# Optimization experiments

Hardware: AMD Instinct MI355X
Metric: run time of the kernel (lower is better)

The kernel has to match this reference:

```python
import jax, jax.numpy as jnp
import numpy as np

NEG = -1e30   # finite stand-in for -inf (keeps vjp NaN-free)
BLANK = 0


def _ctc_loss_mean(logits, targets):
    """CTC loss matching torch.nn.CTCLoss(blank=0, zero_infinity=True,
    reduction='mean') applied to log_softmax(logits).permute(1,0,2), with
    input_lengths = T and uniform target_lengths = L.

    logits:  (B, T, K) raw scores
    targets: (B, L) int labels in [1, K) (no blanks)
    """
    B, T, K = logits.shape
    L = targets.shape[1]
    S = 2 * L + 1  # extended label sequence: blank-interleaved

    logp = jax.nn.log_softmax(logits, axis=-1)  # (B, T, K)

    # extended labels ext = [blank, y1, blank, y2, ..., yL, blank]
    ext = jnp.full((B, S), BLANK, dtype=targets.dtype)
    ext = ext.at[:, 1::2].set(targets)  # (B, S)

    # per-step log-probs of extended labels: lp[b, t, s] = logp[b, t, ext[b, s]]
    lp = jnp.take_along_axis(logp, ext[:, None, :], axis=2)  # (B, T, S)

    # skip transition (s-2 -> s) allowed iff ext[s] != blank and ext[s] != ext[s-2]
    skip = jnp.concatenate(
        [jnp.zeros((B, 2), dtype=bool),
         (ext[:, 2:] != BLANK) & (ext[:, 2:] != ext[:, :-2])], axis=1)  # (B, S)

    # alpha init at t = 0
    alpha0 = jnp.full((B, S), NEG, dtype=logp.dtype)
    alpha0 = alpha0.at[:, 0].set(lp[:, 0, 0]).at[:, 1].set(lp[:, 0, 1])

    pad1 = jnp.full((B, 1), NEG, dtype=logp.dtype)
    pad2 = jnp.full((B, 2), NEG, dtype=logp.dtype)

    def step(alpha, lp_t):
        a1 = alpha                                            # stay
        a2 = jnp.concatenate([pad1, alpha[:, :-1]], axis=1)   # advance 1
        a3 = jnp.concatenate([pad2, alpha[:, :-2]], axis=1)   # advance 2
        a3 = jnp.where(skip, a3, NEG)
        new = jnp.logaddexp(jnp.logaddexp(a1, a2), a3) + lp_t
        return new, None

    xs = jnp.swapaxes(lp[:, 1:, :], 0, 1)  # (T-1, B, S)
    alpha, _ = jax.lax.scan(step, alpha0, xs)

    # total log-likelihood: end at last blank or last label
    logl = jnp.logaddexp(alpha[:, S - 1], alpha[:, S - 2])  # (B,)

    per = -logl / L  # 'mean' reduction divides each loss by target length
    per = jnp.where(logl > -1e29, per, 0.0)  # zero_infinity
    return jnp.mean(per)


def setup_inputs() -> dict:
    key = jax.random.key(0)
    k1, k2 = jax.random.split(key)
    B, T, K, L = 64, 1024, 512, 100
    logits = jax.random.normal(k1, (B, T, K), dtype=jnp.float32)
    targets = jax.random.randint(k2, (B, L), 1, K)  # labels exclude blank=0
    return {"logits": logits, "targets": targets}


def reference(logits, targets):
    return _ctc_loss_mean(logits, targets)
```

## Files before the change

kernel.cpp:

```cpp
#include <hip/hip_runtime.h>
#include <hip/hip_fp16.h>


#define TT 1024
#define BB 64
#define KK 512
#define LL 100

static constexpr float L2E = 1.44269504088896340736f;
static constexpr float LN2 = 0.69314718055994530942f;

__device__ __forceinline__ float dpp_shr1_z(float x) {
  return __builtin_bit_cast(float,
      __builtin_amdgcn_update_dpp(0, __builtin_bit_cast(int, x),
                                  0x138, 0xf, 0xf, true));
}
__device__ __forceinline__ int dpp_shr1_zi(int x) {
  return __builtin_amdgcn_update_dpp(0, x, 0x138, 0xf, 0xf, true);
}

__device__ __forceinline__ float slog2(float x) {
  return x > 0.0f ? log2f(x) : -1.0e30f;
}

__device__ __forceinline__ float2 upk(unsigned u) {
  return __half22float2(__builtin_bit_cast(__half2, u));
}

__global__ __launch_bounds__(256) void k_probs(const float* __restrict__ logits,
                                               const int* __restrict__ targets,
                                               unsigned* __restrict__ pk,
                                               float* __restrict__ lbArr,
                                               float* __restrict__ out) {
  const int wid = threadIdx.x >> 6;
  const int lane = threadIdx.x & 63;
  const int row = (blockIdx.x << 2) + wid;
  const int b = row >> 10;
  const float* x = logits + (size_t)row * KK;

  if (blockIdx.x == 0 && threadIdx.x == 0) out[0] = 0.0f;

  __shared__ float sx[4][KK];

  const float4 v0 = reinterpret_cast<const float4*>(x)[lane];
  const float4 v1 = reinterpret_cast<const float4*>(x)[lane + 64];
  float4* sp = reinterpret_cast<float4*>(sx[wid]);
  sp[lane] = v0;
  sp[lane + 64] = v1;

  float m = fmaxf(fmaxf(fmaxf(v0.x, v0.y), fmaxf(v0.z, v0.w)),
                  fmaxf(fmaxf(v1.x, v1.y), fmaxf(v1.z, v1.w)));
  #pragma unroll
  for (int d = 1; d < 64; d <<= 1) m = fmaxf(m, __shfl_xor(m, d));

  float e = exp2f((v0.x - m) * L2E) + exp2f((v0.y - m) * L2E) +
            exp2f((v0.z - m) * L2E) + exp2f((v0.w - m) * L2E) +
            exp2f((v1.x - m) * L2E) + exp2f((v1.y - m) * L2E) +
            exp2f((v1.z - m) * L2E) + exp2f((v1.w - m) * L2E);
  #pragma unroll
  for (int d = 1; d < 64; d <<= 1) e += __shfl_xor(e, d);

  __syncthreads();
  const float xb = sx[wid][0];

  float ox = 0.0f, oy = 0.0f;
  if (lane >= 1 && lane <= 50) {
    const int2 c = *reinterpret_cast<const int2*>(
        targets + b * LL + (2 * lane - 2));
    ox = exp2f((sx[wid][c.x] - xb) * L2E);
    oy = exp2f((sx[wid][c.y] - xb) * L2E);
  }
  const int word = (lane == 0) ? 63 : (lane - 1);
  const __half2 h = __floats2half2_rn(ox, oy);
  pk[(size_t)(row >> 1) * 128 + word * 2 + (row & 1)] =
      __builtin_bit_cast(unsigned, h);

  if (lane == 0) lbArr[row] = (xb - m) * L2E + 9.0f - log2f(e);
}

__global__ __launch_bounds__(128) void k_ctc(const unsigned* __restrict__ pk,
                                             const float* __restrict__ lbArr,
                                             const int* __restrict__ targets,
                                             float* __restrict__ out) {
  const int b = blockIdx.x;
  const int lane = threadIdx.x & 63;
  const int wv = threadIdx.x >> 6;
  const int i = lane;
  const int* tg = targets + b * LL;

  __shared__ float sG[6][64];

  float S0 = 0.0f, S1 = 0.0f, S2 = 0.0f, S3 = 0.0f;
  int ea = 0;
  float f1 = 1.0f, f2 = 1.0f;

  const float4* lbv = reinterpret_cast<const float4*>(lbArr + (size_t)b * TT);
  const int lbbase = (wv == 0) ? 0 : 128;
  const float4 lb0 = lbv[lbbase + lane];
  const float4 lb1 = lbv[lbbase + lane + 64];

#define RESC()                                                             \
  do {                                                                     \
    const float m_ = fmaxf(fmaxf(S0, S1), fmaxf(S2, S3));                  \
    int E_ = (int)((__float_as_uint(m_) >> 23) & 255) - 127;               \
    E_ = (m_ > 0.0f) ? E_ : 0;                                             \
    const float sc_ = __uint_as_float((unsigned)(127 - E_) << 23);         \
    S0 *= sc_; S1 *= sc_; S2 *= sc_; S3 *= sc_;                            \
    ea += E_;                                                              \
    int dE_ = dpp_shr1_zi(ea) - ea;                                        \
    dE_ = dE_ < -250 ? -250 : (dE_ > 250 ? 250 : dE_);                     \
    const int h_ = dE_ / 2;                                                \
    f1 = __uint_as_float((unsigned)(127 + h_) << 23);                      \
    f2 = __uint_as_float((unsigned)(127 + (dE_ - h_)) << 23);              \
  } while (0)

  uint2 RA[8], RB[8], RC[8], RD[8], RE[8], RF[8], RG[8], RH[8];

  if (wv == 0) {
    const unsigned* gb = pk + (size_t)b * 512 * 128 + i * 2;
    float mA = 0.0f, mB = 0.0f;
    if (i > 0 && 2 * i <= LL - 1)
      mA = (tg[2 * i] != tg[2 * i - 1]) ? 1.0f : 0.0f;
    if (2 * i + 1 <= LL - 1)
      mB = (tg[2 * i + 1] != tg[2 * i]) ? 1.0f : 0.0f;
    S0 = (i == 0) ? 1.0f : 0.0f;

#define FISSUE(BUF, CHN)                                                   \
    do {                                                                   \
      if ((CHN) < 32) {                                                    \
        _Pragma("unroll") for (int j = 0; j < 8; ++j)                      \
          BUF[j] = *reinterpret_cast<const uint2*>(                        \
              gb + (size_t)((CHN) * 8 + j) * 128);                         \
        __builtin_amdgcn_sched_barrier(0);                                 \
      }                                                                    \
    } while (0)
#define FSTEP(R)                                                           \
    do {                                                                   \
      const float A3 = dpp_shr1_z(S3) * f1 * f2;                           \
      const float n0 = S0 + A3;                                            \
      const float n1 = (S0 + S1 + mA * A3) * (R).x;                        \
      const float n2 = S1 + S2;                                            \
      const float n3 = (S2 + S3 + mB * S1) * (R).y;                        \
      S0 = n0; S1 = n1; S2 = n2; S3 = n3;                                  \
    } while (0)
#define FCOMPUTE(BUF)                                                      \
    do {                                                                   \
      _Pragma("unroll") for (int j = 0; j < 8; ++j) {                      \
        const float2 re = upk(BUF[j].x);                                   \
        FSTEP(re);                                                         \
        const float2 ro = upk(BUF[j].y);                                   \
        FSTEP(ro);                                                         \
        if ((j & 3) == 3) RESC();                       \
      }                                                                    \
    } while (0)

    FISSUE(RA, 0); FISSUE(RB, 1); FISSUE(RC, 2); FISSUE(RD, 3);
    FISSUE(RE, 4); FISSUE(RF, 5); FISSUE(RG, 6);
    for (int c = 0; c < 32; c += 8) {
      FISSUE(RH, c + 7);  FCOMPUTE(RA);
      FISSUE(RA, c + 8);  FCOMPUTE(RB);
      FISSUE(RB, c + 9);  FCOMPUTE(RC);
      FISSUE(RC, c + 10); FCOMPUTE(RD);
      FISSUE(RD, c + 11); FCOMPUTE(RE);
      FISSUE(RE, c + 12); FCOMPUTE(RF);
      FISSUE(RF, c + 13); FCOMPUTE(RG);
      FISSUE(RG, c + 14); FCOMPUTE(RH);
    }
#undef FISSUE
#undef FSTEP
#undef FCOMPUTE
  } else {
    const int ii = 50 - i;
    const int w = (ii >= 0) ? ii : 50;
    const unsigned* gb = pk + (size_t)b * 512 * 128 + w * 2;
    float mBb = 0.0f, mAn = 0.0f;
    if (ii >= 0 && 2 * ii + 1 <= LL - 1)
      mBb = (tg[2 * ii + 1] != tg[2 * ii]) ? 1.0f : 0.0f;
    if (ii >= 0 && ii <= 48)
      mAn = (tg[2 * ii + 2] != tg[2 * ii + 1]) ? 1.0f : 0.0f;
    if (i == 0) S0 = 1.0f;
    if (i == 1) S3 = 1.0f;

#define BISSUE(BUF, CHN)                                                   \
    do {                                                                   \
      if ((CHN) < 32) {                                                    \
        _Pragma("unroll") for (int j = 0; j < 8; ++j)                      \
          BUF[j] = *reinterpret_cast<const uint2*>(                        \
              gb + (size_t)(511 - ((CHN) * 8 + j)) * 128);                 \
        __builtin_amdgcn_sched_barrier(0);                                 \
      }                                                                    \
    } while (0)
#define BSTEP(R)                                                           \
    do {                                                                   \
      const float s2 = dpp_shr1_z((R).x);           \
      const float H0 = dpp_shr1_z(S0) * f1 * f2;                           \
      const float H1 = dpp_shr1_z(S1) * f1 * f2;                           \
      const float u = (R).x * S1;                                          \
      const float v = (R).y * S3;                                          \
      const float n0 = S0 + u;                                             \
      const float n1 = u + fmaf(mBb, v, S2);                               \
      const float n2 = S2 + v;                                             \
      const float n3 = v + fmaf(mAn, s2 * H1, H0);                         \
      S0 = n0; S1 = n1; S2 = n2; S3 = n3;                                  \
    } while (0)
#define BCOMPUTE(BUF)                                                      \
    do {                                                                   \
      _Pragma("unroll") for (int j = 0; j < 8; ++j) {                      \
        const float2 ro = upk(BUF[j].y);                                   \
        BSTEP(ro);                                                         \
        const float2 re = upk(BUF[j].x);                                   \
        BSTEP(re);                                                         \
        if ((j & 3) == 3) RESC();                       \
      }                                                                    \
    } while (0)

    BISSUE(RA, 0); BISSUE(RB, 1); BISSUE(RC, 2); BISSUE(RD, 3);
    BISSUE(RE, 4); BISSUE(RF, 5); BISSUE(RG, 6);
    for (int c = 0; c < 32; c += 8) {
      BISSUE(RH, c + 7);  BCOMPUTE(RA);
      BISSUE(RA, c + 8);  BCOMPUTE(RB);
      BISSUE(RB, c + 9);  BCOMPUTE(RC);
      BISSUE(RC, c + 10); BCOMPUTE(RD);
      BISSUE(RD, c + 11); BCOMPUTE(RE);
      BISSUE(RE, c + 12); BCOMPUTE(RF);
      BISSUE(RF, c + 13); BCOMPUTE(RG);
      BISSUE(RG, c + 14); BCOMPUTE(RH);
    }
#undef BISSUE
#undef BSTEP
#undef BCOMPUTE
  }
#undef RESC

  float s4 = (lb0.x + lb0.y) + (lb0.z + lb0.w) +
             (lb1.x + lb1.y) + (lb1.z + lb1.w);
  #pragma unroll
  for (int d = 1; d < 64; d <<= 1) s4 += __shfl_xor(s4, d);

  if (wv == 1) {
    sG[0][lane] = S0; sG[1][lane] = S1; sG[2][lane] = S2; sG[3][lane] = S3;
    sG[4][lane] = (float)ea;
    if (lane == 0) sG[5][0] = s4;
  }

  __syncthreads();

  if (wv == 0) {
    const int gj = (i <= 50) ? (50 - i) : 63;
    const float eb = sG[4][gj];
    const float eff = (float)ea;
    float w0 = slog2(S0) + eff + slog2(sG[0][gj]) + eb;
    float w1 = slog2(S1) + eff + slog2(sG[1][gj]) + eb;
    float w2 = slog2(S2) + eff + slog2(sG[2][gj]) + eb;
    float w3 = slog2(S3) + eff + slog2(sG[3][gj]) + eb;
    float wm = fmaxf(fmaxf(w0, w1), fmaxf(w2, w3));
    #pragma unroll
    for (int d = 1; d < 64; d <<= 1) wm = fmaxf(wm, __shfl_xor(wm, d));
    float ss = exp2f(w0 - wm) + exp2f(w1 - wm) +
               exp2f(w2 - wm) + exp2f(w3 - wm);
    #pragma unroll
    for (int d = 1; d < 64; d <<= 1) ss += __shfl_xor(ss, d);

    if (i == 0) {
      const float lbsum = s4 + sG[5][0];
      float loss = 0.0f;
      if (wm > -1.0e29f) {
        const float logl2 = wm + log2f(ss) + lbsum - (float)(TT * 9);
        loss = -(logl2 * LN2) / (float)LL;
      }
      atomicAdd(out, loss * (1.0f / (float)BB));
    }
  }
}

extern "C" void kernel_launch(void* const* d_in, const int* in_sizes, int n_in,
                              void* d_out, int out_size, void* d_ws, size_t ws_size,
                              hipStream_t stream) {
  const float* logits = (const float*)d_in[0];
  const int* targets = (const int*)d_in[1];
  float* out = (float*)d_out;

  unsigned* pk = (unsigned*)d_ws;
  float* lbArr = (float*)d_ws + (size_t)BB * 512 * 128;

  hipLaunchKernelGGL(k_probs, dim3(BB * TT / 4), dim3(256), 0, stream,
                     logits, targets, pk, lbArr, out);
  hipLaunchKernelGGL(k_ctc, dim3(BB), dim3(128), 0, stream,
                     pk, lbArr, targets, out);
}
```

Baseline: 51.63 us.

## Split CTC recurrence across kernels to overlap it with middle-row softmax

The single probability kernel and the single recurrence kernel become three. The first computes edge time rows. The middle kernel runs the first 320 forward and backward steps while other blocks compute the softmax for the middle 384 rows. The tail kernel reloads the saved alpha/beta state and finishes the recurrence. This hides part of the serial recurrence behind memory-bound softmax work, at the cost of an extra launch, a state round-trip through global memory, and a shallower 4-buffer prefetch pipeline.

```diff
diff --git a/kernel.cpp b/kernel.cpp
--- a/kernel.cpp
+++ b/kernel.cpp
@@ -6,6 +6,7 @@
 #define BB 64
 #define KK 512
 #define LL 100
+#define DLT 320
 
 static constexpr float L2E = 1.44269504088896340736f;
 static constexpr float LN2 = 0.69314718055994530942f;
@@ -18,35 +19,141 @@
 __device__ __forceinline__ int dpp_shr1_zi(int x) {
   return __builtin_amdgcn_update_dpp(0, x, 0x138, 0xf, 0xf, true);
 }
-
 __device__ __forceinline__ float slog2(float x) {
   return x > 0.0f ? log2f(x) : -1.0e30f;
 }
-
 __device__ __forceinline__ float2 upk(unsigned u) {
   return __half22float2(__builtin_bit_cast(__half2, u));
 }
 
-__global__ __launch_bounds__(256) void k_probs(const float* __restrict__ logits,
-                                               const int* __restrict__ targets,
-                                               unsigned* __restrict__ pk,
-                                               float* __restrict__ lbArr,
-                                               float* __restrict__ out) {
-  const int wid = threadIdx.x >> 6;
-  const int lane = threadIdx.x & 63;
-  const int row = (blockIdx.x << 2) + wid;
-  const int b = row >> 10;
+__device__ __forceinline__ void resc(float& S0, float& S1, float& S2,
+                                     float& S3, int& ea, float& f1,
+                                     float& f2) {
+  const float m = fmaxf(fmaxf(S0, S1), fmaxf(S2, S3));
+  int E = (int)((__float_as_uint(m) >> 23) & 255) - 127;
+  E = (m > 0.0f) ? E : 0;
+  const float sc = __uint_as_float((unsigned)(127 - E) << 23);
+  S0 *= sc; S1 *= sc; S2 *= sc; S3 *= sc;
+  ea += E;
+  int dE = dpp_shr1_zi(ea) - ea;
+  dE = dE < -250 ? -250 : (dE > 250 ? 250 : dE);
+  const int h = dE / 2;
+  f1 = __uint_as_float((unsigned)(127 + h) << 23);
+  f2 = __uint_as_float((unsigned)(127 + (dE - h)) << 23);
+}
+__device__ __forceinline__ void refresh_f(int ea, float& f1, float& f2) {
+  int dE = dpp_shr1_zi(ea) - ea;
+  dE = dE < -250 ? -250 : (dE > 250 ? 250 : dE);
+  const int h = dE / 2;
+  f1 = __uint_as_float((unsigned)(127 + h) << 23);
+  f2 = __uint_as_float((unsigned)(127 + (dE - h)) << 23);
+}
+
+__device__ __forceinline__ void fstep(float2 r, float mA, float mB,
+                                      float& S0, float& S1, float& S2,
+                                      float& S3, float f1, float f2) {
+  const float A3 = dpp_shr1_z(S3) * f1 * f2;
+  const float n0 = S0 + A3;
+  const float n1 = (S0 + S1 + mA * A3) * r.x;
+  const float n2 = S1 + S2;
+  const float n3 = (S2 + S3 + mB * S1) * r.y;
+  S0 = n0; S1 = n1; S2 = n2; S3 = n3;
+}
+__device__ __forceinline__ void bstep(float2 r, float mBb, float mAn,
+                                      float& S0, float& S1, float& S2,
+                                      float& S3, float f1, float f2) {
+  const float s2 = dpp_shr1_z(r.x);
+  const float H0 = dpp_shr1_z(S0) * f1 * f2;
+  const float H1 = dpp_shr1_z(S1) * f1 * f2;
+  const float u = r.x * S1;
+  const float v = r.y * S3;
+  const float n0 = S0 + u;
+  const float n1 = u + fmaf(mBb, v, S2);
+  const float n2 = S2 + v;
+  const float n3 = v + fmaf(mAn, s2 * H1, H0);
+  S0 = n0; S1 = n1; S2 = n2; S3 = n3;
+}
+
+template <int CB, int NC>
+__device__ __forceinline__ void run_fwd(const unsigned* __restrict__ gb,
+                                        float mA, float mB, float& S0,
+                                        float& S1, float& S2, float& S3,
+                                        int& ea, float& f1, float& f2) {
+  uint2 RA[8], RB[8], RC[8], RD[8];
+#define ISSUE(BUF, CHN)                                                    \
+  do {                                                                     \
+    if ((CHN) < NC) {                                                      \
+      _Pragma("unroll") for (int j = 0; j < 8; ++j)                        \
+        BUF[j] = *reinterpret_cast<const uint2*>(                          \
+            gb + (size_t)((CB + (CHN)) * 8 + j) * 128);                    \
+      __builtin_amdgcn_sched_barrier(0);                                   \
+    }                                                                      \
+  } while (0)
+#define COMP(BUF)                                                          \
+  do {                                                                     \
+    _Pragma("unroll") for (int j = 0; j < 8; ++j) {                        \
+      fstep(upk(BUF[j].x), mA, mB, S0, S1, S2, S3, f1, f2);                \
+      fstep(upk(BUF[j].y), mA, mB, S0, S1, S2, S3, f1, f2);                \
+      if ((j & 3) == 3) resc(S0, S1, S2, S3, ea, f1, f2);                  \
+    }                                                                      \
+  } while (0)
+  ISSUE(RA, 0); ISSUE(RB, 1); ISSUE(RC, 2);
+  for (int c = 0; c < NC; c += 4) {
+    ISSUE(RD, c + 3); COMP(RA);
+    ISSUE(RA, c + 4); COMP(RB);
+    ISSUE(RB, c + 5); COMP(RC);
+    ISSUE(RC, c + 6); COMP(RD);
+  }
+#undef ISSUE
+#undef COMP
+}
+
+template <int CB, int NC>
+__device__ __forceinline__ void run_bwd(const unsigned* __restrict__ gb,
+                                        float mBb, float mAn, float& S0,
+                                        float& S1, float& S2, float& S3,
+                                        int& ea, float& f1, float& f2) {
+  uint2 RA[8], RB[8], RC[8], RD[8];
+#define ISSUE(BUF, CHN)                                                    \
+  do {                                                                     \
+    if ((CHN) < NC) {                                                      \
+      _Pragma("unroll") for (int j = 0; j < 8; ++j)                        \
+        BUF[j] = *reinterpret_cast<const uint2*>(                          \
+            gb + (size_t)(511 - ((CB + (CHN)) * 8 + j)) * 128);            \
+      __builtin_amdgcn_sched_barrier(0);                                   \
+    }                                                                      \
+  } while (0)
+#define COMP(BUF)                                                          \
+  do {                                                                     \
+    _Pragma("unroll") for (int j = 0; j < 8; ++j) {                        \
+      bstep(upk(BUF[j].y), mBb, mAn, S0, S1, S2, S3, f1, f2);              \
+      bstep(upk(BUF[j].x), mBb, mAn, S0, S1, S2, S3, f1, f2);              \
+      if ((j & 3) == 3) resc(S0, S1, S2, S3, ea, f1, f2);                  \
+    }                                                                      \
+  } while (0)
+  ISSUE(RA, 0); ISSUE(RB, 1); ISSUE(RC, 2);
+  for (int c = 0; c < NC; c += 4) {
+    ISSUE(RD, c + 3); COMP(RA);
+    ISSUE(RA, c + 4); COMP(RB);
+    ISSUE(RB, c + 5); COMP(RC);
+    ISSUE(RC, c + 6); COMP(RD);
+  }
+#undef ISSUE
+#undef COMP
+}
+
+__device__ __forceinline__ void prob_row(const float* __restrict__ logits,
+                                         const int* __restrict__ targets,
+                                         unsigned* __restrict__ pk,
+                                         float* __restrict__ lbArr,
+                                         int b, int t, int lane, float* sp) {
+  const int row = (b << 10) + t;
   const float* x = logits + (size_t)row * KK;
-
-  if (blockIdx.x == 0 && threadIdx.x == 0) out[0] = 0.0f;
-
-  __shared__ float sx[4][KK];
-
   const float4 v0 = reinterpret_cast<const float4*>(x)[lane];
   const float4 v1 = reinterpret_cast<const float4*>(x)[lane + 64];
-  float4* sp = reinterpret_cast<float4*>(sx[wid]);
-  sp[lane] = v0;
-  sp[lane + 64] = v1;
+  float4* sp4 = reinterpret_cast<float4*>(sp);
+  sp4[lane] = v0;
+  sp4[lane + 64] = v1;
 
   float m = fmaxf(fmaxf(fmaxf(v0.x, v0.y), fmaxf(v0.z, v0.w)),
                   fmaxf(fmaxf(v1.x, v1.y), fmaxf(v1.z, v1.w)));
@@ -61,116 +168,73 @@
   for (int d = 1; d < 64; d <<= 1) e += __shfl_xor(e, d);
 
   __syncthreads();
-  const float xb = sx[wid][0];
+  const float xb = sp[0];
 
   float ox = 0.0f, oy = 0.0f;
   if (lane >= 1 && lane <= 50) {
     const int2 c = *reinterpret_cast<const int2*>(
         targets + b * LL + (2 * lane - 2));
-    ox = exp2f((sx[wid][c.x] - xb) * L2E);
-    oy = exp2f((sx[wid][c.y] - xb) * L2E);
+    ox = exp2f((sp[c.x] - xb) * L2E);
+    oy = exp2f((sp[c.y] - xb) * L2E);
   }
   const int word = (lane == 0) ? 63 : (lane - 1);
   const __half2 h = __floats2half2_rn(ox, oy);
   pk[(size_t)(row >> 1) * 128 + word * 2 + (row & 1)] =
       __builtin_bit_cast(unsigned, h);
-
   if (lane == 0) lbArr[row] = (xb - m) * L2E + 9.0f - log2f(e);
 }
 
-__global__ __launch_bounds__(128) void k_ctc(const unsigned* __restrict__ pk,
-                                             const float* __restrict__ lbArr,
-                                             const int* __restrict__ targets,
-                                             float* __restrict__ out) {
-  const int b = blockIdx.x;
+__global__ __launch_bounds__(256) void k_probs_edge(
+    const float* __restrict__ logits, const int* __restrict__ targets,
+    unsigned* __restrict__ pk, float* __restrict__ lbArr,
+    float* __restrict__ out) {
+  if (blockIdx.x == 0 && threadIdx.x == 0) out[0] = 0.0f;
+  const int wid = threadIdx.x >> 6;
+  const int lane = threadIdx.x & 63;
+  __shared__ float sx[4][KK];
+  const int e = (blockIdx.x << 2) + wid;
+  const int b = e / 640;
+  const int w = e - b * 640;
+  const int t = (w < DLT) ? w : (TT - 640) + w;
+  prob_row(logits, targets, pk, lbArr, b, t, lane, sx[wid]);
+}
+
+__global__ __launch_bounds__(256) void k_mid(
+    const float* __restrict__ logits, const int* __restrict__ targets,
+    unsigned* __restrict__ pk, float* __restrict__ lbArr,
+    float* __restrict__ st) {
   const int lane = threadIdx.x & 63;
   const int wv = threadIdx.x >> 6;
-  const int i = lane;
+  __shared__ float sx[4][KK];
+
+  if (blockIdx.x >= BB) {
+    const int m = ((blockIdx.x - BB) << 2) + wv;
+    const int b = m / 384;
+    const int w = m - b * 384;
+    prob_row(logits, targets, pk, lbArr, b, DLT + w, lane, sx[wv]);
+    return;
+  }
+
+  if (wv >= 2) return;
+  const int b = blockIdx.x;
+  const int dir = wv;
   const int* tg = targets + b * LL;
-
-  __shared__ float sG[6][64];
 
   float S0 = 0.0f, S1 = 0.0f, S2 = 0.0f, S3 = 0.0f;
   int ea = 0;
   float f1 = 1.0f, f2 = 1.0f;
 
-  const float4* lbv = reinterpret_cast<const float4*>(lbArr + (size_t)b * TT);
-  const int lbbase = (wv == 0) ? 0 : 128;
-  const float4 lb0 = lbv[lbbase + lane];
-  const float4 lb1 = lbv[lbbase + lane + 64];
-
-#define RESC()                                                             \
-  do {                                                                     \
-    const float m_ = fmaxf(fmaxf(S0, S1), fmaxf(S2, S3));                  \
-    int E_ = (int)((__float_as_uint(m_) >> 23) & 255) - 127;               \
-    E_ = (m_ > 0.0f) ? E_ : 0;                                             \
-    const float sc_ = __uint_as_float((unsigned)(127 - E_) << 23);         \
-    S0 *= sc_; S1 *= sc_; S2 *= sc_; S3 *= sc_;                            \
-    ea += E_;                                                              \
-    int dE_ = dpp_shr1_zi(ea) - ea;                                        \
-    dE_ = dE_ < -250 ? -250 : (dE_ > 250 ? 250 : dE_);                     \
-    const int h_ = dE_ / 2;                                                \
-    f1 = __uint_as_float((unsigned)(127 + h_) << 23);                      \
-    f2 = __uint_as_float((unsigned)(127 + (dE_ - h_)) << 23);              \
-  } while (0)
-
-  uint2 RA[8], RB[8], RC[8], RD[8], RE[8], RF[8], RG[8], RH[8];
-
-  if (wv == 0) {
-    const unsigned* gb = pk + (size_t)b * 512 * 128 + i * 2;
+  if (dir == 0) {
+    const unsigned* gb = pk + (size_t)b * 512 * 128 + lane * 2;
     float mA = 0.0f, mB = 0.0f;
-    if (i > 0 && 2 * i <= LL - 1)
-      mA = (tg[2 * i] != tg[2 * i - 1]) ? 1.0f : 0.0f;
-    if (2 * i + 1 <= LL - 1)
-      mB = (tg[2 * i + 1] != tg[2 * i]) ? 1.0f : 0.0f;
-    S0 = (i == 0) ? 1.0f : 0.0f;
-
-#define FISSUE(BUF, CHN)                                                   \
-    do {                                                                   \
-      if ((CHN) < 32) {                                                    \
-        _Pragma("unroll") for (int j = 0; j < 8; ++j)                      \
-          BUF[j] = *reinterpret_cast<const uint2*>(                        \
-              gb + (size_t)((CHN) * 8 + j) * 128);                         \
-        __builtin_amdgcn_sched_barrier(0);                                 \
-      }                                                                    \
-    } while (0)
-#define FSTEP(R)                                                           \
-    do {                                                                   \
-      const float A3 = dpp_shr1_z(S3) * f1 * f2;                           \
-      const float n0 = S0 + A3;                                            \
-      const float n1 = (S0 + S1 + mA * A3) * (R).x;                        \
-      const float n2 = S1 + S2;                                            \
-      const float n3 = (S2 + S3 + mB * S1) * (R).y;                        \
-      S0 = n0; S1 = n1; S2 = n2; S3 = n3;                                  \
-    } while (0)
-#define FCOMPUTE(BUF)                                                      \
-    do {                                                                   \
-      _Pragma("unroll") for (int j = 0; j < 8; ++j) {                      \
-        const float2 re = upk(BUF[j].x);                                   \
-        FSTEP(re);                                                         \
-        const float2 ro = upk(BUF[j].y);                                   \
-        FSTEP(ro);                                                         \
-        if ((j & 3) == 3) RESC();                       \
-      }                                                                    \
-    } while (0)
-
-    FISSUE(RA, 0); FISSUE(RB, 1); FISSUE(RC, 2); FISSUE(RD, 3);
-    FISSUE(RE, 4); FISSUE(RF, 5); FISSUE(RG, 6);
-    for (int c = 0; c < 32; c += 8) {
-      FISSUE(RH, c + 7);  FCOMPUTE(RA);
-      FISSUE(RA, c + 8);  FCOMPUTE(RB);
-      FISSUE(RB, c + 9);  FCOMPUTE(RC);
-      FISSUE(RC, c + 10); FCOMPUTE(RD);
-      FISSUE(RD, c + 11); FCOMPUTE(RE);
-      FISSUE(RE, c + 12); FCOMPUTE(RF);
-      FISSUE(RF, c + 13); FCOMPUTE(RG);
-      FISSUE(RG, c + 14); FCOMPUTE(RH);
-    }
-#undef FISSUE
-#undef FSTEP
-#undef FCOMPUTE
+    if (lane > 0 && 2 * lane <= LL - 1)
+      mA = (tg[2 * lane] != tg[2 * lane - 1]) ? 1.0f : 0.0f;
+    if (2 * lane + 1 <= LL - 1)
+      mB = (tg[2 * lane + 1] != tg[2 * lane]) ? 1.0f : 0.0f;
+    S0 = (lane == 0) ? 1.0f : 0.0f;
+    run_fwd<0, 20>(gb, mA, mB, S0, S1, S2, S3, ea, f1, f2);
   } else {
-    const int ii = 50 - i;
+    const int ii = 50 - lane;
     const int w = (ii >= 0) ? ii : 50;
     const unsigned* gb = pk + (size_t)b * 512 * 128 + w * 2;
     float mBb = 0.0f, mAn = 0.0f;
@@ -178,75 +242,79 @@
       mBb = (tg[2 * ii + 1] != tg[2 * ii]) ? 1.0f : 0.0f;
     if (ii >= 0 && ii <= 48)
       mAn = (tg[2 * ii + 2] != tg[2 * ii + 1]) ? 1.0f : 0.0f;
-    if (i == 0) S0 = 1.0f;
-    if (i == 1) S3 = 1.0f;
-
-#define BISSUE(BUF, CHN)                                                   \
-    do {                                                                   \
-      if ((CHN) < 32) {                                                    \
-        _Pragma("unroll") for (int j = 0; j < 8; ++j)                      \
-          BUF[j] = *reinterpret_cast<const uint2*>(                        \
-              gb + (size_t)(511 - ((CHN) * 8 + j)) * 128);                 \
-        __builtin_amdgcn_sched_barrier(0);                                 \
-      }                                                                    \
-    } while (0)
-#define BSTEP(R)                                                           \
-    do {                                                                   \
-      const float s2 = dpp_shr1_z((R).x);           \
-      const float H0 = dpp_shr1_z(S0) * f1 * f2;                           \
-      const float H1 = dpp_shr1_z(S1) * f1 * f2;                           \
-      const float u = (R).x * S1;                                          \
-      const float v = (R).y * S3;                                          \
-      const float n0 = S0 + u;                                             \
-      const float n1 = u + fmaf(mBb, v, S2);                               \
-      const float n2 = S2 + v;                                             \
-      const float n3 = v + fmaf(mAn, s2 * H1, H0);                         \
-      S0 = n0; S1 = n1; S2 = n2; S3 = n3;                                  \
-    } while (0)
-#define BCOMPUTE(BUF)                                                      \
-    do {                                                                   \
-      _Pragma("unroll") for (int j = 0; j < 8; ++j) {                      \
-        const float2 ro = upk(BUF[j].y);                                   \
-        BSTEP(ro);                                                         \
-        const float2 re = upk(BUF[j].x);                                   \
-        BSTEP(re);                                                         \
-        if ((j & 3) == 3) RESC();                       \
-      }                                                                    \
-    } while (0)
-
-    BISSUE(RA, 0); BISSUE(RB, 1); BISSUE(RC, 2); BISSUE(RD, 3);
-    BISSUE(RE, 4); BISSUE(RF, 5); BISSUE(RG, 6);
-    for (int c = 0; c < 32; c += 8) {
-      BISSUE(RH, c + 7);  BCOMPUTE(RA);
-      BISSUE(RA, c + 8);  BCOMPUTE(RB);
-      BISSUE(RB, c + 9);  BCOMPUTE(RC);
-      BISSUE(RC, c + 10); BCOMPUTE(RD);
-      BISSUE(RD, c + 11); BCOMPUTE(RE);
-      BISSUE(RE, c + 12); BCOMPUTE(RF);
-      BISSUE(RF, c + 13); BCOMPUTE(RG);
-      BISSUE(RG, c + 14); BCOMPUTE(RH);
-    }
-#undef BISSUE
-#undef BSTEP
-#undef BCOMPUTE
-  }
-#undef RESC
+    if (lane == 0) S0 = 1.0f;
+    if (lane == 1) S3 = 1.0f;
+    run_bwd<0, 20>(gb, mBb, mAn, S0, S1, S2, S3, ea, f1, f2);
+  }
+
+  float* stp = st + (size_t)(b * 2 + dir) * 5 * 64;
+  stp[0 * 64 + lane] = S0;
+  stp[1 * 64 + lane] = S1;
+  stp[2 * 64 + lane] = S2;
+  stp[3 * 64 + lane] = S3;
+  stp[4 * 64 + lane] = __int_as_float(ea);
+}
+
+__global__ __launch_bounds__(128) void k_tail(
+    const unsigned* __restrict__ pk, const float* __restrict__ lbArr,
+    const int* __restrict__ targets, const float* __restrict__ st,
+    float* __restrict__ out) {
+  const int lane = threadIdx.x & 63;
+  const int wv = threadIdx.x >> 6;
+  const int b = blockIdx.x;
+  const int dir = wv;
+  const int* tg = targets + b * LL;
+
+  __shared__ float sG[6][64];
+
+  const float4* lbv = reinterpret_cast<const float4*>(lbArr + (size_t)b * TT);
+  const int lbbase = (dir == 0) ? 0 : 128;
+  const float4 lb0 = lbv[lbbase + lane];
+  const float4 lb1 = lbv[lbbase + lane + 64];
+
+  const float* stp = st + (size_t)(b * 2 + dir) * 5 * 64;
+  float S0 = stp[0 * 64 + lane];
+  float S1 = stp[1 * 64 + lane];
+  float S2 = stp[2 * 64 + lane];
+  float S3 = stp[3 * 64 + lane];
+  int ea = __float_as_int(stp[4 * 64 + lane]);
+  float f1, f2;
+  refresh_f(ea, f1, f2);
+
+  if (dir == 0) {
+    const unsigned* gb = pk + (size_t)b * 512 * 128 + lane * 2;
+    float mA = 0.0f, mB = 0.0f;
+    if (lane > 0 && 2 * lane <= LL - 1)
+      mA = (tg[2 * lane] != tg[2 * lane - 1]) ? 1.0f : 0.0f;
+    if (2 * lane + 1 <= LL - 1)
+      mB = (tg[2 * lane + 1] != tg[2 * lane]) ? 1.0f : 0.0f;
+    run_fwd<20, 12>(gb, mA, mB, S0, S1, S2, S3, ea, f1, f2);
+  } else {
+    const int ii = 50 - lane;
+    const int w = (ii >= 0) ? ii : 50;
+    const unsigned* gb = pk + (size_t)b * 512 * 128 + w * 2;
+    float mBb = 0.0f, mAn = 0.0f;
+    if (ii >= 0 && 2 * ii + 1 <= LL - 1)
+      mBb = (tg[2 * ii + 1] != tg[2 * ii]) ? 1.0f : 0.0f;
+    if (ii >= 0 && ii <= 48)
+      mAn = (tg[2 * ii + 2] != tg[2 * ii + 1]) ? 1.0f : 0.0f;
+    run_bwd<20, 12>(gb, mBb, mAn, S0, S1, S2, S3, ea, f1, f2);
+  }
 
   float s4 = (lb0.x + lb0.y) + (lb0.z + lb0.w) +
              (lb1.x + lb1.y) + (lb1.z + lb1.w);
   #pragma unroll
   for (int d = 1; d < 64; d <<= 1) s4 += __shfl_xor(s4, d);
 
-  if (wv == 1) {
+  if (dir == 1) {
     sG[0][lane] = S0; sG[1][lane] = S1; sG[2][lane] = S2; sG[3][lane] = S3;
     sG[4][lane] = (float)ea;
     if (lane == 0) sG[5][0] = s4;
   }
-
   __syncthreads();
 
-  if (wv == 0) {
-    const int gj = (i <= 50) ? (50 - i) : 63;
+  if (dir == 0) {
+    const int gj = (lane <= 50) ? (50 - lane) : 63;
     const float eb = sG[4][gj];
     const float eff = (float)ea;
     float w0 = slog2(S0) + eff + slog2(sG[0][gj]) + eb;
@@ -261,7 +329,7 @@
     #pragma unroll
     for (int d = 1; d < 64; d <<= 1) ss += __shfl_xor(ss, d);
 
-    if (i == 0) {
+    if (lane == 0) {
       const float lbsum = s4 + sG[5][0];
       float loss = 0.0f;
       if (wm > -1.0e29f) {
@@ -282,9 +350,12 @@
 
   unsigned* pk = (unsigned*)d_ws;
   float* lbArr = (float*)d_ws + (size_t)BB * 512 * 128;
-
-  hipLaunchKernelGGL(k_probs, dim3(BB * TT / 4), dim3(256), 0, stream,
+  float* st = lbArr + (size_t)BB * TT;
+
+  hipLaunchKernelGGL(k_probs_edge, dim3(BB * 640 / 4), dim3(256), 0, stream,
                      logits, targets, pk, lbArr, out);
-  hipLaunchKernelGGL(k_ctc, dim3(BB), dim3(128), 0, stream,
-                     pk, lbArr, targets, out);
-}
+  hipLaunchKernelGGL(k_mid, dim3(BB + BB * 384 / 4), dim3(256), 0, stream,
+                     logits, targets, pk, lbArr, st);
+  hipLaunchKernelGGL(k_tail, dim3(BB), dim3(128), 0, stream,
+                     pk, lbArr, targets, st, out);
+}
```

Result: faster. 47.85 us (-7.3%).
